# Performance work log

Hardware: AMD Instinct MI355X
Metric: run time of the kernel (lower is better)

The kernel has to match this reference:

```python
import jax, jax.numpy as jnp
import numpy as np

B, NB, C, FEAT = 2, 512, 80, 1024
FIRST_N = 128
NMS_FC = 128
POS_EMB = 64
GROUPS = 16
ATT_D = (1024, 1024, 128)
NUM_THRESH = 3
BBOX_W = (10.0, 10.0, 5.0, 5.0)
SCALE_CLAMP = float(np.log(1000.0 / 16.0))


def setup_inputs() -> dict:
    key = jax.random.key(0)
    ks = jax.random.split(key, 24)
    roi_feat = jax.random.normal(ks[0], (B * NB, FEAT), jnp.float32)
    scores = jax.random.normal(ks[1], (B * NB, C + 1), jnp.float32)
    proposal_deltas = jax.random.normal(ks[2], (B * NB, C * 4), jnp.float32) * 0.5
    xy = jax.random.uniform(ks[3], (B * NB, 2), jnp.float32) * 800.0
    wh = jax.random.uniform(ks[4], (B * NB, 2), jnp.float32) * 100.0 + 1.0
    proposal_boxes = jnp.concatenate([xy, xy + wh], axis=1)

    def lin(k, fin, fout, std=0.01):
        return jax.random.normal(k, (fin, fout), jnp.float32) * std

    return {
        'roi_feat': roi_feat,
        'scores': scores,
        'proposal_deltas': proposal_deltas,
        'proposal_boxes': proposal_boxes,
        'roi_w': lin(ks[5], FEAT, NMS_FC), 'roi_b': jnp.zeros((NMS_FC,), jnp.float32),
        'rank_w': lin(ks[6], FEAT, NMS_FC), 'rank_b': jnp.zeros((NMS_FC,), jnp.float32),
        'logit_w': lin(ks[7], NMS_FC, NUM_THRESH), 'logit_b': jnp.full((NUM_THRESH,), -3.0, jnp.float32),
        'pos_w': lin(ks[8], POS_EMB, GROUPS), 'pos_b': jnp.zeros((GROUPS,), jnp.float32),
        'q_w': lin(ks[9], NMS_FC, ATT_D[0]), 'q_b': jnp.zeros((ATT_D[0],), jnp.float32),
        'k_w': lin(ks[10], NMS_FC, ATT_D[1]), 'k_b': jnp.zeros((ATT_D[1],), jnp.float32),
        'out_w': jax.random.normal(ks[11], (GROUPS, NMS_FC, ATT_D[2] // GROUPS), jnp.float32) * 0.01,
        'out_b': jnp.zeros((ATT_D[2],), jnp.float32),
        'num_boxes': NB,
    }


def _rank_embedding():
    # sinusoidal rank embedding, dim FEAT
    fr = jnp.arange(FEAT // 2, dtype=jnp.float32)
    dim_mat = jnp.power(1000.0, (2.0 / FEAT) * fr)
    div = jnp.arange(FIRST_N, dtype=jnp.float32)[:, None] / dim_mat[None, :]
    return jnp.concatenate([jnp.sin(div), jnp.cos(div)], axis=1)  # (FIRST_N, FEAT)


def _pos_embed(boxes):
    # boxes: (FIRST_N, C, 4) -> (C, N, N, POS_EMB)
    b = jnp.transpose(boxes, (1, 0, 2))  # (C, N, 4)
    x1, y1, x2, y2 = b[..., 0], b[..., 1], b[..., 2], b[..., 3]
    w = x2 - x1 + 1.0
    h = y2 - y1 + 1.0
    cx = 0.5 * (x1 + x2)
    cy = 0.5 * (y1 + y2)
    dx = jnp.log(jnp.maximum(jnp.abs((cx[:, :, None] - cx[:, None, :]) / w[:, :, None]), 1e-3))
    dy = jnp.log(jnp.maximum(jnp.abs((cy[:, :, None] - cy[:, None, :]) / h[:, :, None]), 1e-3))
    dw = jnp.log(w[:, :, None] / w[:, None, :])
    dh = jnp.log(h[:, :, None] / h[:, None, :])
    pm = jnp.stack([dx, dy, dw, dh], axis=-1)  # (C, N, N, 4)
    fr = jnp.arange(POS_EMB // 8, dtype=jnp.float32)
    dim_mat = jnp.power(1000.0, (8.0 / POS_EMB) * fr)
    dv = (pm * 100.0)[..., None] / dim_mat  # (C, N, N, 4, POS_EMB//8)
    e = jnp.concatenate([jnp.sin(dv), jnp.cos(dv)], axis=-1)  # (C, N, N, 4, POS_EMB//4)
    return e.reshape(pm.shape[:3] + (POS_EMB,))


def reference(roi_feat, scores, proposal_deltas, proposal_boxes,
              roi_w, roi_b, rank_w, rank_b, logit_w, logit_b,
              pos_w, pos_b, q_w, q_b, k_w, k_b, out_w, out_b, num_boxes):
    deltas = jax.lax.stop_gradient(proposal_deltas)  # detached in original
    pboxes = jax.lax.stop_gradient(proposal_boxes)
    batch = deltas.shape[0] // num_boxes

    # ---- Box2BoxTransform.apply_deltas ----
    widths = pboxes[:, 2] - pboxes[:, 0]
    heights = pboxes[:, 3] - pboxes[:, 1]
    ctr_x = pboxes[:, 0] + 0.5 * widths
    ctr_y = pboxes[:, 1] + 0.5 * heights
    wx, wy, ww, wh = BBOX_W
    d = deltas.reshape(-1, C, 4)
    dx = d[..., 0] / wx
    dy = d[..., 1] / wy
    dw = jnp.minimum(d[..., 2] / ww, SCALE_CLAMP)
    dh = jnp.minimum(d[..., 3] / wh, SCALE_CLAMP)
    pcx = dx * widths[:, None] + ctr_x[:, None]
    pcy = dy * heights[:, None] + ctr_y[:, None]
    pw = jnp.exp(dw) * widths[:, None]
    ph = jnp.exp(dh) * heights[:, None]
    refined = jnp.stack([pcx - 0.5 * pw, pcy - 0.5 * ph, pcx + 0.5 * pw, pcy + 0.5 * ph], axis=-1)
    refined = refined.reshape(batch, num_boxes, C, 4)

    # ---- softmax + per-class descending sort, keep first_n ----
    sc = scores.reshape(batch, num_boxes, C + 1)
    probs = jax.nn.softmax(sc[..., :C], axis=1)
    rank_idxs = jnp.argsort(-probs, axis=1)[:, :FIRST_N, :]  # (B, FIRST_N, C)
    sorted_score = jnp.take_along_axis(probs, rank_idxs, axis=1)  # (B, FIRST_N, C)
    sorted_boxes = jax.vmap(lambda bx, i: jnp.take_along_axis(bx, i[..., None], axis=0))(refined, rank_idxs)  # (B, FIRST_N, C, 4)

    # ---- rank + roi embeddings ----
    rank_feat = _rank_embedding() @ rank_w + rank_b  # (FIRST_N, NMS_FC)
    roi_emb = (roi_feat @ roi_w + roi_b).reshape(batch, num_boxes, NMS_FC)
    sorted_roi = jax.vmap(lambda e, i: e[i])(roi_emb, rank_idxs)  # (B, FIRST_N, C, NMS_FC)
    emb_feat = sorted_roi + rank_feat[None, :, None, :]

    dq = ATT_D[0] // GROUPS
    dk = ATT_D[1] // GROUPS

    def attend(feat, boxes):
        # feat: (FIRST_N, C, NMS_FC), boxes: (FIRST_N, C, 4)
        pe = _pos_embed(boxes)  # (C, N, N, POS_EMB)
        aff_w = jax.nn.relu(pe @ pos_w + pos_b)  # (C, N, N, G)
        aff_w = jnp.transpose(aff_w, (0, 3, 1, 2))  # (C, G, N, N)
        f = jnp.transpose(feat, (1, 0, 2))  # (C, N, NMS_FC)
        q = (f @ q_w + q_b).reshape(C, FIRST_N, GROUPS, dq).transpose(0, 2, 1, 3)
        k = (f @ k_w + k_b).reshape(C, FIRST_N, GROUPS, dk).transpose(0, 2, 1, 3)
        aff = jnp.einsum('cgnd,cgmd->cgnm', q, k) / jnp.sqrt(jnp.float32(dk))
        sm = jax.nn.softmax(jnp.log(jnp.maximum(aff_w, 1e-6)) + aff, axis=-1)
        ov = jnp.einsum('cgnm,cmd->cgnd', sm, f)  # (C, G, N, NMS_FC)
        lin = jnp.einsum('cgnd,gde->cnge', ov, out_w).reshape(C, FIRST_N, ATT_D[2]) + out_b
        return jnp.transpose(lin, (1, 0, 2))  # (N, C, ATT_D[2])

    att = jax.vmap(attend)(emb_feat, sorted_boxes)
    all_feat = jax.nn.relu(emb_feat + att)
    logit = all_feat @ logit_w + logit_b  # (B, FIRST_N, C, NUM_THRESH)
    nms_multi_score = jax.nn.sigmoid(logit) * sorted_score[..., None]
    return nms_multi_score
```

## Files before the change

kernel.cpp:

```cpp
#include <hip/hip_runtime.h>
#include <math.h>

#define B_    2
#define NB_   512
#define C_    80
#define FEAT_ 1024
#define FN_   128
#define FC_   128
#define PE_   64
#define G_    16
#define DQ_   64
#define EO_   8
#define NT_   3
#define SCALE_CLAMP_ 4.135166556742356f

typedef __attribute__((ext_vector_type(8))) short bf16x8;
typedef __attribute__((ext_vector_type(4))) float f32x4;

#define O_ROIP    ((size_t)0)
#define O_RANKP   (O_ROIP + (size_t)2*B_*NB_*FC_)
#define O_RANKIDX (O_RANKP + (size_t)2*FN_*FC_)
#define O_SSCORE  (O_RANKIDX + (size_t)B_*FN_*C_)
#define O_SBOX    (O_SSCORE + (size_t)B_*FN_*C_)
#define O_EMB     (O_SBOX + (size_t)B_*FN_*C_*4)
#define O_ATT     (O_EMB + (size_t)B_*FN_*C_*FC_)
#define O_LW      (O_ATT + (size_t)B_*FN_*C_*FC_)
#define O_WT      (O_LW + (size_t)B_*C_*FN_*G_*FN_/2)
#define O_EMBB    (O_WT + (size_t)16*144*128/2)

__device__ __forceinline__ float bf2f(unsigned short u) {
    return __uint_as_float(((unsigned int)u) << 16);
}
__device__ __forceinline__ unsigned short f2bf(float f) {
    unsigned int x = __float_as_uint(f);
    unsigned int r = (x + 0x7fff + ((x >> 16) & 1)) >> 16;
    return (unsigned short)r;
}
__device__ __forceinline__ unsigned short f2h(float x) {
    _Float16 h = (_Float16)x;
    return __builtin_bit_cast(unsigned short, h);
}
__device__ __forceinline__ float h2f(unsigned short u) {
    _Float16 h = __builtin_bit_cast(_Float16, u);
    return (float)h;
}

#define ADDR128(row, gr)  ((row)*128 + ((((gr) ^ ((row)&7))) << 4))

__global__ __launch_bounds__(256) void k_prep(const float* __restrict__ q_w,
                                              const float* __restrict__ k_w,
                                              const float* __restrict__ out_w,
                                              unsigned short* __restrict__ wt)
{
    const int g = blockIdx.x;
    const int t = threadIdx.x;
    for (int idx = t; idx < 144*16; idx += 256) {
        const int row = idx >> 4;
        const int kc  = (idx & 15) * 8;
        unsigned short u[8];
        if (row < 64) {
            #pragma unroll
            for (int j = 0; j < 8; ++j) u[j] = f2bf(q_w[(size_t)(kc + j)*1024 + g*DQ_ + row]);
        } else if (row < 128) {
            const int r = row - 64;
            #pragma unroll
            for (int j = 0; j < 8; ++j) u[j] = f2bf(k_w[(size_t)(kc + j)*1024 + g*DQ_ + r]);
        } else if (row < 136) {
            const int e = row - 128;
            #pragma unroll
            for (int j = 0; j < 8; ++j) u[j] = f2bf(out_w[(size_t)g*FC_*EO_ + (size_t)(kc + j)*EO_ + e]);
        } else {
            #pragma unroll
            for (int j = 0; j < 8; ++j) u[j] = 0;
        }
        *(uint4*)(wt + (size_t)g*144*128 + row*128 + kc) =
            make_uint4((unsigned)u[0] | ((unsigned)u[1] << 16),
                       (unsigned)u[2] | ((unsigned)u[3] << 16),
                       (unsigned)u[4] | ((unsigned)u[5] << 16),
                       (unsigned)u[6] | ((unsigned)u[7] << 16));
    }
}

__global__ __launch_bounds__(256) void k_embed(const float* __restrict__ roi_feat,
                                               const float* __restrict__ roi_w,
                                               const float* __restrict__ roi_b,
                                               const float* __restrict__ rank_w,
                                               const float* __restrict__ rank_b,
                                               float* __restrict__ roiP,
                                               float* __restrict__ rankP)
{
    const int bid = blockIdx.x;
    const int kh  = bid & 1;
    const int rt  = bid >> 1;
    const bool isRank = rt >= 64;
    const int row0 = (isRank ? rt - 64 : rt) * 16;
    const int t = threadIdx.x;
    const int w = t >> 6, lane = t & 63, lr = lane & 15, lh = lane >> 4;
    const int col0 = w * 32;
    const float* W = isRank ? rank_w : roi_w;
    const float* bias = isRank ? rank_b : roi_b;

    const int arow = row0 + lr;
    f32x4 acc0 = {0,0,0,0}, acc1 = {0,0,0,0};

    #pragma unroll 4
    for (int ks = 0; ks < 16; ++ks) {
        const int kb = kh*512 + ks*32 + lh*8;
        bf16x8 af;
        if (!isRank) {
            float4 a0 = *(const float4*)(roi_feat + (size_t)arow*FEAT_ + kb);
            float4 a1 = *(const float4*)(roi_feat + (size_t)arow*FEAT_ + kb + 4);
            af[0] = (short)f2bf(a0.x); af[1] = (short)f2bf(a0.y);
            af[2] = (short)f2bf(a0.z); af[3] = (short)f2bf(a0.w);
            af[4] = (short)f2bf(a1.x); af[5] = (short)f2bf(a1.y);
            af[6] = (short)f2bf(a1.z); af[7] = (short)f2bf(a1.w);
        } else {
            #pragma unroll
            for (int j = 0; j < 8; ++j) {
                int k = kb + j;
                int kk = k & 511;
                float inv = exp2f(-(float)kk * 0.0194644226f);
                float arg = (float)arow * inv;
                float v = (k < 512) ? __sinf(arg) : __cosf(arg);
                af[j] = (short)f2bf(v);
            }
        }
        bf16x8 bf0, bf1;
        #pragma unroll
        for (int j = 0; j < 8; ++j) {
            const float* wr = W + (size_t)(kb + j)*FC_ + col0 + lr;
            bf0[j] = (short)f2bf(wr[0]);
            bf1[j] = (short)f2bf(wr[16]);
        }
        acc0 = __builtin_amdgcn_mfma_f32_16x16x32_bf16(af, bf0, acc0, 0, 0, 0);
        acc1 = __builtin_amdgcn_mfma_f32_16x16x32_bf16(af, bf1, acc1, 0, 0, 0);
    }
    float* dst = isRank ? (rankP + (size_t)kh*FN_*FC_) : (roiP + (size_t)kh*(B_*NB_)*FC_);
    #pragma unroll
    for (int tile = 0; tile < 2; ++tile) {
        f32x4 a = tile ? acc1 : acc0;
        int col = col0 + tile*16 + lr;
        float bv = (kh == 0) ? bias[col] : 0.0f;
        #pragma unroll
        for (int reg = 0; reg < 4; ++reg) {
            int rr = row0 + lh*4 + reg;
            dst[(size_t)rr*FC_ + col] = a[reg] + bv;
        }
    }
}

__global__ __launch_bounds__(512) void k_topk(const float* __restrict__ scores,
                                              int* __restrict__ rank_idx,
                                              float* __restrict__ sorted_score)
{
    int b = blockIdx.x / C_, c = blockIdx.x % C_;
    __shared__ float p[NB_];
    __shared__ float red[NB_];
    int i = threadIdx.x;
    float s = scores[(size_t)(b*NB_ + i)*(C_+1) + c];
    red[i] = s; __syncthreads();
    for (int o = 256; o > 0; o >>= 1) { if (i < o) red[i] = fmaxf(red[i], red[i+o]); __syncthreads(); }
    float mx = red[0]; __syncthreads();
    float e = expf(s - mx);
    red[i] = e; __syncthreads();
    for (int o = 256; o > 0; o >>= 1) { if (i < o) red[i] += red[i+o]; __syncthreads(); }
    float sum = red[0]; __syncthreads();
    float pi = e / sum;
    p[i] = pi; __syncthreads();
    int rank = 0;
    for (int j4 = 0; j4 < NB_/4; ++j4) {
        float4 pj = *(const float4*)&p[j4*4];
        int j = j4*4;
        rank += (pj.x > pi) || (pj.x == pi && (j+0) < i);
        rank += (pj.y > pi) || (pj.y == pi && (j+1) < i);
        rank += (pj.z > pi) || (pj.z == pi && (j+2) < i);
        rank += (pj.w > pi) || (pj.w == pi && (j+3) < i);
    }
    if (rank < FN_) {
        rank_idx[(size_t)(b*FN_ + rank)*C_ + c] = i;
        sorted_score[(size_t)(b*FN_ + rank)*C_ + c] = pi;
    }
}

__global__ __launch_bounds__(256) void k_gather(const int* __restrict__ rank_idx,
                                                const float* __restrict__ roiP,
                                                const float* __restrict__ rankP,
                                                const float* __restrict__ pdeltas,
                                                const float* __restrict__ pboxes,
                                                float* __restrict__ emb_feat,
                                                unsigned short* __restrict__ embB,
                                                float* __restrict__ sorted_boxes)
{
    const int t = threadIdx.x;
    const int item = blockIdx.x*8 + (t >> 5);
    const int l = t & 31;
    const int c = item % C_;
    const int bn = item / C_;
    const int n = bn & (FN_-1);
    const int b = bn >> 7;
    const int idx = rank_idx[item];
    const int row = b*NB_ + idx;
    float4 e0 = *(const float4*)(roiP + (size_t)row*FC_ + l*4);
    float4 e1 = *(const float4*)(roiP + (size_t)(B_*NB_ + row)*FC_ + l*4);
    float4 r0 = *(const float4*)(rankP + (size_t)n*FC_ + l*4);
    float4 r1 = *(const float4*)(rankP + (size_t)(FN_ + n)*FC_ + l*4);
    float4 sm = make_float4(e0.x+e1.x+r0.x+r1.x, e0.y+e1.y+r0.y+r1.y,
                            e0.z+e1.z+r0.z+r1.z, e0.w+e1.w+r0.w+r1.w);
    *(float4*)(emb_feat + (size_t)item*FC_ + l*4) = sm;
    *(uint2*)(embB + (size_t)item*FC_ + l*4) =
        make_uint2((unsigned)f2bf(sm.x) | ((unsigned)f2bf(sm.y) << 16),
                   (unsigned)f2bf(sm.z) | ((unsigned)f2bf(sm.w) << 16));
    if (l == 0) {
        float x1 = pboxes[row*4+0], y1 = pboxes[row*4+1], x2 = pboxes[row*4+2], y2 = pboxes[row*4+3];
        float w = x2 - x1, h = y2 - y1;
        float cx = x1 + 0.5f*w, cy = y1 + 0.5f*h;
        const float* dl = pdeltas + (size_t)row*(C_*4) + c*4;
        float dx = dl[0]/10.0f, dy = dl[1]/10.0f;
        float dw = fminf(dl[2]/5.0f, SCALE_CLAMP_);
        float dh = fminf(dl[3]/5.0f, SCALE_CLAMP_);
        float pcx = dx*w + cx, pcy = dy*h + cy;
        float pw = expf(dw)*w, ph = expf(dh)*h;
        float* ob = sorted_boxes + (size_t)item*4;
        ob[0] = pcx - 0.5f*pw; ob[1] = pcy - 0.5f*ph;
        ob[2] = pcx + 0.5f*pw; ob[3] = pcy + 0.5f*ph;
    }
}

__global__ __launch_bounds__(256) void k_pos2(const float* __restrict__ sorted_boxes,
                                              const float* __restrict__ pos_w,
                                              const float* __restrict__ pos_b,
                                              unsigned short* __restrict__ lw)
{
    const int n2   = blockIdx.x & 63;
    const int rest = blockIdx.x >> 6;
    const int cl   = rest % C_;
    const int b    = rest / C_;
    const int n0   = n2 * 2;
    const int t    = threadIdx.x;

    __shared__ float geomL[FN_][6];
    __shared__ unsigned short featL[256*PE_];
    __shared__ unsigned short poswL[G_*PE_];
    __shared__ float pbL[G_];
    __shared__ float sdimL[8];

    if (t < FN_) {
        const float* bx = sorted_boxes + (((size_t)(b*FN_ + t))*C_ + cl)*4;
        float x1 = bx[0], y1 = bx[1], x2 = bx[2], y2 = bx[3];
        float w = x2 - x1 + 1.0f;
        float h = y2 - y1 + 1.0f;
        geomL[t][0] = 0.5f*(x1+x2);
        geomL[t][1] = 0.5f*(y1+y2);
        geomL[t][2] = w;
        geomL[t][3] = h;
        geomL[t][4] = __logf(w);
        geomL[t][5] = __logf(h);
    } else {
        int id = t - 128;
        int g  = id >> 3;
        int gr = id & 7;
        unsigned short u[8];
        #pragma unroll
        for (int j = 0; j < 8; ++j) u[j] = f2bf(pos_w[(gr*8 + j)*G_ + g]);
        *(uint4*)((char*)poswL + ADDR128(g, gr)) =
            make_uint4((unsigned)u[0] | ((unsigned)u[1] << 16),
                       (unsigned)u[2] | ((unsigned)u[3] << 16),
                       (unsigned)u[4] | ((unsigned)u[5] << 16),
                       (unsigned)u[6] | ((unsigned)u[7] << 16));
    }
    if (t < G_) pbL[t] = pos_b[t];
    if (t >= 16 && t < 24) sdimL[t-16] = 1.0f / powf(1000.0f, 0.125f*(float)(t-16));
    __syncthreads();

    {
        const int nl = t >> 7;
        const int m  = t & 127;
        const int n  = n0 + nl;
        float pm[4];
        {
            float cxn = geomL[n][0], cyn = geomL[n][1];
            float rwn = 1.0f/geomL[n][2], rhn = 1.0f/geomL[n][3];
            pm[0] = __logf(fmaxf(fabsf((cxn - geomL[m][0]) * rwn), 1e-3f)) * 100.0f;
            pm[1] = __logf(fmaxf(fabsf((cyn - geomL[m][1]) * rhn), 1e-3f)) * 100.0f;
            pm[2] = (geomL[n][4] - geomL[m][4]) * 100.0f;
            pm[3] = (geomL[n][5] - geomL[m][5]) * 100.0f;
        }
        char* base = (char*)featL;
        #pragma unroll
        for (int f = 0; f < 4; ++f) {
            float s[8], c[8];
            #pragma unroll
            for (int r = 0; r < 8; ++r) {
                __sincosf(pm[f] * sdimL[r], &s[r], &c[r]);
            }
            unsigned short us[8], uc[8];
            #pragma unroll
            for (int r = 0; r < 8; ++r) { us[r] = f2bf(s[r]); uc[r] = f2bf(c[r]); }
            *(uint4*)(base + ADDR128(t, 2*f)) =
                make_uint4((unsigned)us[0] | ((unsigned)us[1] << 16),
                           (unsigned)us[2] | ((unsigned)us[3] << 16),
                           (unsigned)us[4] | ((unsigned)us[5] << 16),
                           (unsigned)us[6] | ((unsigned)us[7] << 16));
            *(uint4*)(base + ADDR128(t, 2*f + 1)) =
                make_uint4((unsigned)uc[0] | ((unsigned)uc[1] << 16),
                           (unsigned)uc[2] | ((unsigned)uc[3] << 16),
                           (unsigned)uc[4] | ((unsigned)uc[5] << 16),
                           (unsigned)uc[6] | ((unsigned)uc[7] << 16));
        }
    }
    __syncthreads();

    {
        const int wave = t >> 6, lane = t & 63;
        const int lr = lane & 15, lh = lane >> 4;
        const float pbg = pbL[lr];
        #pragma unroll
        for (int ti = 0; ti < 4; ++ti) {
            const int t16 = wave*4 + ti;
            f32x4 acc = {0,0,0,0};
            #pragma unroll
            for (int ks = 0; ks < 2; ++ks) {
                bf16x8 a  = *(const bf16x8*)((char*)featL + ADDR128(t16*16 + lr, ks*4 + lh));
                bf16x8 bb = *(const bf16x8*)((char*)poswL + ADDR128(lr, ks*4 + lh));
                acc = __builtin_amdgcn_mfma_f32_16x16x32_bf16(a, bb, acc, 0, 0, 0);
            }
            const int g = lr;
            #pragma unroll
            for (int reg = 0; reg < 4; ++reg) {
                int p = t16*16 + lh*4 + reg;
                int n = n0 + (p >> 7);
                int m = p & 127;
                float w = fmaxf(fmaxf(acc[reg] + pbg, 0.0f), 1e-6f);
                lw[(((size_t)(b*C_ + cl)*FN_ + n)*G_ + g)*FN_ + m] = f2h(__logf(w));
            }
        }
    }
}

#define FT_OFF   0
#define QL_OFF   34816
#define KL_OFF   51200
#define VT_OFF   67584
#define BIAS_OFF 71680
#define SMEM_SZ  72192

__global__ __launch_bounds__(1024, 8) void k_attn(const unsigned short* __restrict__ embB,
                                               const unsigned short* __restrict__ wt,
                                               const float* __restrict__ q_b,
                                               const float* __restrict__ k_b,
                                               const float* __restrict__ out_b,
                                               const unsigned short* __restrict__ lw,
                                               float* __restrict__ att)
{
    const int g    = blockIdx.x & 15;
    const int rest = blockIdx.x >> 4;
    const int cl   = rest % C_;
    const int b    = rest / C_;
    const int c    = cl;
    const int t  = threadIdx.x;
    const int wave = t >> 6;
    const int lane = t & 63;
    const int lr = lane & 15;
    const int lh = lane >> 4;

    __shared__ char smem[SMEM_SZ];
    float* biasL = (float*)(smem + BIAS_OFF);

    {
        const char* src = (const char*)embB + ((size_t)(b*FN_)*C_ + c)*FC_*2;
        #pragma unroll
        for (int s = 0; s < 2; ++s) {
            int fi = t + s*1024;
            int n  = fi >> 4;
            int o16 = (fi & 15) * 16;
            uint4 v = *(const uint4*)(src + (size_t)n*C_*FC_*2 + o16);
            *(uint4*)(smem + FT_OFF + n*272 + o16) = v;
        }
    }
    if (t >= 512 && t < 768) {
        int i = t - 512;
        *(uint2*)(smem + VT_OFF + 8*256 + i*8) = make_uint2(0u, 0u);
    }
    if (t >= 128 && t < 256) {
        int r = t - 128;
        biasL[r] = (r < 64) ? q_b[g*DQ_ + r] : k_b[g*DQ_ + (r-64)];
    }
    __syncthreads();

    {
        const int rb = (wave >> 2) * 32;
        const int nb = (wave & 3) * 32;
        const char* wtg = (const char*)wt + (size_t)g*144*256;
        f32x4 acc00 = {0,0,0,0}, acc01 = {0,0,0,0}, acc10 = {0,0,0,0}, acc11 = {0,0,0,0};
        f32x4 accV  = {0,0,0,0};
        #pragma unroll
        for (int ks = 0; ks < 4; ++ks) {
            const int fo = ks*64 + lh*16;
            bf16x8 a0 = *(const bf16x8*)(wtg + (rb + lr)*256 + fo);
            bf16x8 a1 = *(const bf16x8*)(wtg + (rb + 16 + lr)*256 + fo);
            bf16x8 b0 = *(const bf16x8*)(smem + FT_OFF + (nb + lr)*272 + fo);
            bf16x8 b1 = *(const bf16x8*)(smem + FT_OFF + (nb + 16 + lr)*272 + fo);
            acc00 = __builtin_amdgcn_mfma_f32_16x16x32_bf16(a0, b0, acc00, 0, 0, 0);
            acc01 = __builtin_amdgcn_mfma_f32_16x16x32_bf16(a0, b1, acc01, 0, 0, 0);
            acc10 = __builtin_amdgcn_mfma_f32_16x16x32_bf16(a1, b0, acc10, 0, 0, 0);
            acc11 = __builtin_amdgcn_mfma_f32_16x16x32_bf16(a1, b1, acc11, 0, 0, 0);
            if (wave < 8) {
                bf16x8 av = *(const bf16x8*)(wtg + (128 + lr)*256 + fo);
                bf16x8 bv = *(const bf16x8*)(smem + FT_OFF + (wave*16 + lr)*272 + fo);
                accV = __builtin_amdgcn_mfma_f32_16x16x32_bf16(av, bv, accV, 0, 0, 0);
            }
        }
        #pragma unroll
        for (int ti = 0; ti < 2; ++ti) {
            #pragma unroll
            for (int tj = 0; tj < 2; ++tj) {
                f32x4 a = (ti == 0) ? (tj == 0 ? acc00 : acc01) : (tj == 0 ? acc10 : acc11);
                int r0 = rb + ti*16 + lh*4;
                int n  = nb + tj*16 + lr;
                float v0 = a[0] + biasL[r0+0];
                float v1 = a[1] + biasL[r0+1];
                float v2 = a[2] + biasL[r0+2];
                float v3 = a[3] + biasL[r0+3];
                int dq0 = r0 & 63;
                int off = (r0 < 64 ? QL_OFF : KL_OFF);
                char* dst = smem + off + ADDR128(n, dq0 >> 3) + ((dq0 >> 2) & 1)*8;
                *(uint2*)dst = make_uint2((unsigned)f2bf(v0) | ((unsigned)f2bf(v1) << 16),
                                          (unsigned)f2bf(v2) | ((unsigned)f2bf(v3) << 16));
            }
        }
        if (wave < 8 && lh < 2) {
            int m = wave*16 + lr;
            #pragma unroll
            for (int reg = 0; reg < 4; ++reg) {
                int e = lh*4 + reg;
                char* dst = smem + VT_OFF + (e)*256 + ((((m >> 3) ^ e)) << 4) + (m & 7)*2;
                *(unsigned short*)dst = f2bf(accV[reg]);
            }
        }
    }
    __syncthreads();

    {
        const int nb = (wave >> 2) * 32;
        const int mb = (wave & 3) * 32;
        f32x4 acc00 = {0,0,0,0}, acc01 = {0,0,0,0}, acc10 = {0,0,0,0}, acc11 = {0,0,0,0};
        #pragma unroll
        for (int ks = 0; ks < 2; ++ks) {
            int soff = ((ks*4 + lh) ^ (lr & 7)) << 4;
            bf16x8 a0 = *(const bf16x8*)(smem + QL_OFF + (nb + lr)*128 + soff);
            bf16x8 a1 = *(const bf16x8*)(smem + QL_OFF + (nb + 16 + lr)*128 + soff);
            bf16x8 b0 = *(const bf16x8*)(smem + KL_OFF + (mb + lr)*128 + soff);
            bf16x8 b1 = *(const bf16x8*)(smem + KL_OFF + (mb + 16 + lr)*128 + soff);
            acc00 = __builtin_amdgcn_mfma_f32_16x16x32_bf16(a0, b0, acc00, 0, 0, 0);
            acc01 = __builtin_amdgcn_mfma_f32_16x16x32_bf16(a0, b1, acc01, 0, 0, 0);
            acc10 = __builtin_amdgcn_mfma_f32_16x16x32_bf16(a1, b0, acc10, 0, 0, 0);
            acc11 = __builtin_amdgcn_mfma_f32_16x16x32_bf16(a1, b1, acc11, 0, 0, 0);
        }
        #pragma unroll
        for (int ti = 0; ti < 2; ++ti) {
            #pragma unroll
            for (int tj = 0; tj < 2; ++tj) {
                f32x4 a = (ti == 0) ? (tj == 0 ? acc00 : acc01) : (tj == 0 ? acc10 : acc11);
                int n0 = nb + ti*16 + lh*4;
                int m  = mb + tj*16 + lr;
                #pragma unroll
                for (int reg = 0; reg < 4; ++reg)
                    *(unsigned short*)(smem + FT_OFF + (n0 + reg)*272 + 2*m) = f2h(a[reg]);
            }
        }
    }
    __syncthreads();

    {
        const int row = t >> 3;
        const int lp  = t & 7;
        const int m0  = lp * 16;
        const unsigned short* lwrow = lw + ((((size_t)(b*C_ + cl))*FN_ + row)*G_ + g)*FN_ + m0;
        uint4 gl0 = *(const uint4*)(lwrow);
        uint4 gl1 = *(const uint4*)(lwrow + 8);
        char* abase = smem + FT_OFF + row*272 + lp*32;
        uint4 af0 = *(const uint4*)abase;
        uint4 af1 = *(const uint4*)(abase + 16);
        const unsigned short* ah0 = (const unsigned short*)&af0;
        const unsigned short* ah1 = (const unsigned short*)&af1;
        const unsigned short* lp0 = (const unsigned short*)&gl0;
        const unsigned short* lp1 = (const unsigned short*)&gl1;
        float v[16];
        float mx = -INFINITY;
        #pragma unroll
        for (int j = 0; j < 8; ++j) {
            float val = h2f(ah0[j])*0.125f + h2f(lp0[j]);
            v[j] = val; mx = fmaxf(mx, val);
        }
        #pragma unroll
        for (int j = 0; j < 8; ++j) {
            float val = h2f(ah1[j])*0.125f + h2f(lp1[j]);
            v[8+j] = val; mx = fmaxf(mx, val);
        }
        #pragma unroll
        for (int s = 1; s < 8; s <<= 1) mx = fmaxf(mx, __shfl_xor(mx, s, 8));
        float sum = 0.f;
        #pragma unroll
        for (int j = 0; j < 16; ++j) { v[j] = __expf(v[j] - mx); sum += v[j]; }
        #pragma unroll
        for (int s = 1; s < 8; s <<= 1) sum += __shfl_xor(sum, s, 8);
        float rs = 1.0f / sum;
        unsigned short u[16];
        #pragma unroll
        for (int j = 0; j < 16; ++j) u[j] = f2bf(v[j] * rs);
        *(uint4*)abase = make_uint4((unsigned)u[0] | ((unsigned)u[1] << 16),
                                    (unsigned)u[2] | ((unsigned)u[3] << 16),
                                    (unsigned)u[4] | ((unsigned)u[5] << 16),
                                    (unsigned)u[6] | ((unsigned)u[7] << 16));
        *(uint4*)(abase + 16) = make_uint4((unsigned)u[8]  | ((unsigned)u[9]  << 16),
                                           (unsigned)u[10] | ((unsigned)u[11] << 16),
                                           (unsigned)u[12] | ((unsigned)u[13] << 16),
                                           (unsigned)u[14] | ((unsigned)u[15] << 16));
    }
    __syncthreads();

    if (wave < 8) {
        const int tb = wave * 16;
        f32x4 acc = {0,0,0,0};
        #pragma unroll
        for (int ks = 0; ks < 4; ++ks) {
            const int fo = ks*64 + lh*16;
            int soff = ((ks*4 + lh) ^ lr) << 4;
            bf16x8 a = *(const bf16x8*)(smem + FT_OFF + (tb + lr)*272 + fo);
            bf16x8 bv = *(const bf16x8*)(smem + VT_OFF + lr*256 + soff);
            acc = __builtin_amdgcn_mfma_f32_16x16x32_bf16(a, bv, acc, 0, 0, 0);
        }
        if (lr < 8) {
            float ob = out_b[g*EO_ + lr];
            #pragma unroll
            for (int reg = 0; reg < 4; ++reg) {
                int n = tb + lh*4 + reg;
                att[((size_t)(b*FN_ + n)*C_ + c)*FC_ + g*EO_ + lr] = acc[reg] + ob;
            }
        }
    }
}

__global__ __launch_bounds__(256) void k_final(const float* __restrict__ emb_feat,
                                               const float* __restrict__ att,
                                               const float* __restrict__ logit_w,
                                               const float* __restrict__ logit_b,
                                               const float* __restrict__ sorted_score,
                                               float* __restrict__ out)
{
    __shared__ float lwL[FC_*NT_ + NT_];
    const int t = threadIdx.x;
    for (int i = t; i < FC_*NT_ + NT_; i += 256)
        lwL[i] = (i < FC_*NT_) ? logit_w[i] : logit_b[i - FC_*NT_];
    __syncthreads();
    const int item = blockIdx.x*8 + (t >> 5);
    const int l = t & 31;
    const int d0 = l*4;
    float4 ev = *(const float4*)(emb_feat + (size_t)item*FC_ + d0);
    float4 av = *(const float4*)(att + (size_t)item*FC_ + d0);
    float a0 = fmaxf(ev.x + av.x, 0.f);
    float a1 = fmaxf(ev.y + av.y, 0.f);
    float a2 = fmaxf(ev.z + av.z, 0.f);
    float a3 = fmaxf(ev.w + av.w, 0.f);
    float s0 = a0*lwL[(d0+0)*NT_+0] + a1*lwL[(d0+1)*NT_+0] + a2*lwL[(d0+2)*NT_+0] + a3*lwL[(d0+3)*NT_+0];
    float s1 = a0*lwL[(d0+0)*NT_+1] + a1*lwL[(d0+1)*NT_+1] + a2*lwL[(d0+2)*NT_+1] + a3*lwL[(d0+3)*NT_+1];
    float s2 = a0*lwL[(d0+0)*NT_+2] + a1*lwL[(d0+1)*NT_+2] + a2*lwL[(d0+2)*NT_+2] + a3*lwL[(d0+3)*NT_+2];
    #pragma unroll
    for (int s = 1; s < 32; s <<= 1) {
        s0 += __shfl_xor(s0, s, 32);
        s1 += __shfl_xor(s1, s, 32);
        s2 += __shfl_xor(s2, s, 32);
    }
    if (l < NT_) {
        float lg = (l == 0) ? s0 : (l == 1) ? s1 : s2;
        lg += lwL[FC_*NT_ + l];
        float sg = 1.f / (1.f + expf(-lg));
        out[(size_t)item*NT_ + l] = sg * sorted_score[item];
    }
}

extern "C" void kernel_launch(void* const* d_in, const int* in_sizes, int n_in,
                              void* d_out, int out_size, void* d_ws, size_t ws_size,
                              hipStream_t stream) {
    (void)in_sizes; (void)n_in; (void)out_size; (void)ws_size;
    const float* roi_feat = (const float*)d_in[0];
    const float* scores   = (const float*)d_in[1];
    const float* pdeltas  = (const float*)d_in[2];
    const float* pboxes   = (const float*)d_in[3];
    const float* roi_w    = (const float*)d_in[4];
    const float* roi_b    = (const float*)d_in[5];
    const float* rank_w   = (const float*)d_in[6];
    const float* rank_b   = (const float*)d_in[7];
    const float* logit_w  = (const float*)d_in[8];
    const float* logit_b  = (const float*)d_in[9];
    const float* pos_w    = (const float*)d_in[10];
    const float* pos_b    = (const float*)d_in[11];
    const float* q_w      = (const float*)d_in[12];
    const float* q_b      = (const float*)d_in[13];
    const float* k_w      = (const float*)d_in[14];
    const float* k_b      = (const float*)d_in[15];
    const float* out_w    = (const float*)d_in[16];
    const float* out_b    = (const float*)d_in[17];
    float* ws = (float*)d_ws;

    float* roiP         = ws + O_ROIP;
    float* rankP        = ws + O_RANKP;
    int*   rank_idx     = (int*)(ws + O_RANKIDX);
    float* sorted_score = ws + O_SSCORE;
    float* sorted_boxes = ws + O_SBOX;
    float* emb_feat     = ws + O_EMB;
    float* att          = ws + O_ATT;
    unsigned short* lwb = (unsigned short*)(ws + O_LW);
    unsigned short* wtb = (unsigned short*)(ws + O_WT);
    unsigned short* embB = (unsigned short*)(ws + O_EMBB);

    k_prep<<<dim3(G_), dim3(256), 0, stream>>>(q_w, k_w, out_w, wtb);
    k_embed<<<dim3(144), dim3(256), 0, stream>>>(roi_feat, roi_w, roi_b, rank_w, rank_b,
                                                 roiP, rankP);
    k_topk<<<dim3(B_*C_), dim3(512), 0, stream>>>(scores, rank_idx, sorted_score);
    k_gather<<<dim3(B_*FN_*C_/8), dim3(256), 0, stream>>>(rank_idx, roiP, rankP,
                                                          pdeltas, pboxes, emb_feat, embB, sorted_boxes);
    k_pos2<<<dim3(B_*C_*64), dim3(256), 0, stream>>>(sorted_boxes, pos_w, pos_b, lwb);
    k_attn<<<dim3(B_*C_*G_), dim3(1024), 0, stream>>>(embB, wtb, q_b, k_b, out_b, lwb, att);
    k_final<<<dim3(B_*FN_*C_/8), dim3(256), 0, stream>>>(emb_feat, att, logit_w, logit_b,
                                                         sorted_score, d_out ? (float*)d_out : nullptr);
}
```

Measured before the change: 195.7 us.

## Fuse weight prep into embed kernel, reorder attention grid, prefetch pos-weights early

The separate k_prep launch is folded into k_embed as 16 extra blocks, which removes one kernel launch and lets the weight conversion run alongside the embedding GEMM. The k_attn block index now puts the group index outermost, so blocks that run at the same time share the same group weights. The per-thread load of the positional log-weight rows is moved to the start of k_attn so its global-memory latency overlaps the earlier shared-memory and MFMA stages, at the cost of holding eight more registers live through the kernel.

```diff
diff --git a/kernel.cpp b/kernel.cpp
--- a/kernel.cpp
+++ b/kernel.cpp
@@ -47,54 +47,53 @@
 
 #define ADDR128(row, gr)  ((row)*128 + ((((gr) ^ ((row)&7))) << 4))
 
-__global__ __launch_bounds__(256) void k_prep(const float* __restrict__ q_w,
-                                              const float* __restrict__ k_w,
-                                              const float* __restrict__ out_w,
-                                              unsigned short* __restrict__ wt)
-{
-    const int g = blockIdx.x;
-    const int t = threadIdx.x;
-    for (int idx = t; idx < 144*16; idx += 256) {
-        const int row = idx >> 4;
-        const int kc  = (idx & 15) * 8;
-        unsigned short u[8];
-        if (row < 64) {
-            #pragma unroll
-            for (int j = 0; j < 8; ++j) u[j] = f2bf(q_w[(size_t)(kc + j)*1024 + g*DQ_ + row]);
-        } else if (row < 128) {
-            const int r = row - 64;
-            #pragma unroll
-            for (int j = 0; j < 8; ++j) u[j] = f2bf(k_w[(size_t)(kc + j)*1024 + g*DQ_ + r]);
-        } else if (row < 136) {
-            const int e = row - 128;
-            #pragma unroll
-            for (int j = 0; j < 8; ++j) u[j] = f2bf(out_w[(size_t)g*FC_*EO_ + (size_t)(kc + j)*EO_ + e]);
-        } else {
-            #pragma unroll
-            for (int j = 0; j < 8; ++j) u[j] = 0;
-        }
-        *(uint4*)(wt + (size_t)g*144*128 + row*128 + kc) =
-            make_uint4((unsigned)u[0] | ((unsigned)u[1] << 16),
-                       (unsigned)u[2] | ((unsigned)u[3] << 16),
-                       (unsigned)u[4] | ((unsigned)u[5] << 16),
-                       (unsigned)u[6] | ((unsigned)u[7] << 16));
-    }
-}
-
 __global__ __launch_bounds__(256) void k_embed(const float* __restrict__ roi_feat,
                                                const float* __restrict__ roi_w,
                                                const float* __restrict__ roi_b,
                                                const float* __restrict__ rank_w,
                                                const float* __restrict__ rank_b,
+                                               const float* __restrict__ q_w,
+                                               const float* __restrict__ k_w,
+                                               const float* __restrict__ out_w,
                                                float* __restrict__ roiP,
-                                               float* __restrict__ rankP)
+                                               float* __restrict__ rankP,
+                                               unsigned short* __restrict__ wtg)
 {
     const int bid = blockIdx.x;
+    const int t = threadIdx.x;
+    if (bid >= 144) {
+        const int g = bid - 144;
+        for (int idx = t; idx < 144*16; idx += 256) {
+            const int row = idx >> 4;
+            const int kc  = (idx & 15) * 8;
+            unsigned short u[8];
+            if (row < 64) {
+                #pragma unroll
+                for (int j = 0; j < 8; ++j) u[j] = f2bf(q_w[(size_t)(kc + j)*1024 + g*DQ_ + row]);
+            } else if (row < 128) {
+                const int r = row - 64;
+                #pragma unroll
+                for (int j = 0; j < 8; ++j) u[j] = f2bf(k_w[(size_t)(kc + j)*1024 + g*DQ_ + r]);
+            } else if (row < 136) {
+                const int e = row - 128;
+                #pragma unroll
+                for (int j = 0; j < 8; ++j) u[j] = f2bf(out_w[(size_t)g*FC_*EO_ + (size_t)(kc + j)*EO_ + e]);
+            } else {
+                #pragma unroll
+                for (int j = 0; j < 8; ++j) u[j] = 0;
+            }
+            *(uint4*)(wtg + (size_t)g*144*128 + row*128 + kc) =
+                make_uint4((unsigned)u[0] | ((unsigned)u[1] << 16),
+                           (unsigned)u[2] | ((unsigned)u[3] << 16),
+                           (unsigned)u[4] | ((unsigned)u[5] << 16),
+                           (unsigned)u[6] | ((unsigned)u[7] << 16));
+        }
+        return;
+    }
     const int kh  = bid & 1;
     const int rt  = bid >> 1;
     const bool isRank = rt >= 64;
     const int row0 = (isRank ? rt - 64 : rt) * 16;
-    const int t = threadIdx.x;
     const int w = t >> 6, lane = t & 63, lr = lane & 15, lh = lane >> 4;
     const int col0 = w * 32;
     const float* W = isRank ? rank_w : roi_w;
@@ -352,10 +351,10 @@
                                                const unsigned short* __restrict__ lw,
                                                float* __restrict__ att)
 {
-    const int g    = blockIdx.x & 15;
-    const int rest = blockIdx.x >> 4;
-    const int cl   = rest % C_;
-    const int b    = rest / C_;
+    const int bc   = blockIdx.x % (B_*C_);
+    const int g    = blockIdx.x / (B_*C_);
+    const int cl   = bc % C_;
+    const int b    = bc / C_;
     const int c    = cl;
     const int t  = threadIdx.x;
     const int wave = t >> 6;
@@ -365,6 +364,15 @@
 
     __shared__ char smem[SMEM_SZ];
     float* biasL = (float*)(smem + BIAS_OFF);
+
+    uint4 gl0, gl1;
+    {
+        const int row_p = t >> 3;
+        const int lp_p  = t & 7;
+        const unsigned short* lwrow = lw + (((size_t)bc*FN_ + row_p)*G_ + g)*FN_ + lp_p*16;
+        gl0 = *(const uint4*)(lwrow);
+        gl1 = *(const uint4*)(lwrow + 8);
+    }
 
     {
         const char* src = (const char*)embB + ((size_t)(b*FN_)*C_ + c)*FC_*2;
@@ -474,10 +482,6 @@
     {
         const int row = t >> 3;
         const int lp  = t & 7;
-        const int m0  = lp * 16;
-        const unsigned short* lwrow = lw + ((((size_t)(b*C_ + cl))*FN_ + row)*G_ + g)*FN_ + m0;
-        uint4 gl0 = *(const uint4*)(lwrow);
-        uint4 gl1 = *(const uint4*)(lwrow + 8);
         char* abase = smem + FT_OFF + row*272 + lp*32;
         uint4 af0 = *(const uint4*)abase;
         uint4 af1 = *(const uint4*)(abase + 16);
@@ -614,9 +618,8 @@
     unsigned short* wtb = (unsigned short*)(ws + O_WT);
     unsigned short* embB = (unsigned short*)(ws + O_EMBB);
 
-    k_prep<<<dim3(G_), dim3(256), 0, stream>>>(q_w, k_w, out_w, wtb);
-    k_embed<<<dim3(144), dim3(256), 0, stream>>>(roi_feat, roi_w, roi_b, rank_w, rank_b,
-                                                 roiP, rankP);
+    k_embed<<<dim3(160), dim3(256), 0, stream>>>(roi_feat, roi_w, roi_b, rank_w, rank_b,
+                                                 q_w, k_w, out_w, roiP, rankP, wtb);
     k_topk<<<dim3(B_*C_), dim3(512), 0, stream>>>(scores, rank_idx, sorted_score);
     k_gather<<<dim3(B_*FN_*C_/8), dim3(256), 0, stream>>>(rank_idx, roiP, rankP,
                                                           pdeltas, pboxes, emb_feat, embB, sorted_boxes);
```

Measured after the change: 194.7 us. Within noise of the previous version (-0.5%).
